# Kernel tuning notes

Measured on AMD Instinct MI355X. Metric: run time of the kernel, lower is better.

## Reference

```python
import jax, jax.numpy as jnp
import numpy as np

B, N, F, H, OUT, K, L = 32, 2048, 3, 64, 128, 16, 3


def _edge_mlp(e, w1, b1, wo, bo):
    # Faithful to the given MLP.forward: layer1 -> ReLU -> output (layer2 is skipped!)
    return jax.nn.relu(e @ w1 + b1) @ wo + bo


def _dynamic_edge_conv(x, k, w1, b1, wo, bo):
    # x: [B, N, D]. kNN in feature space (self included, distance 0), per graph.
    sq = jnp.sum(x * x, axis=-1)                                   # [B, N]
    d2 = sq[:, :, None] + sq[:, None, :] - 2.0 * jnp.einsum('bnd,bmd->bnm', x, x)
    _, idx = jax.lax.top_k(-d2, k)                                 # [B, N, K]
    x_j = jax.vmap(lambda xb, ib: xb[ib])(x, idx)                  # [B, N, K, D] gather
    x_i = jnp.broadcast_to(x[:, :, None, :], x_j.shape)
    e = jnp.concatenate([x_i, x_j - x_i], axis=-1)                 # EdgeConv message [B,N,K,2D]
    h = _edge_mlp(e, w1, b1, wo, bo)                               # [B, N, K, H]
    return jnp.mean(h, axis=2)                                     # aggr='mean' -> [B, N, H]


def setup_inputs() -> dict:
    key = jax.random.key(0)
    ks = jax.random.split(key, 20)
    inp = {'x': jax.random.normal(ks[0], (B, N, F), dtype=jnp.float32)}
    kit = iter(ks[1:])
    for i in range(L):
        din = 2 * F if i == 0 else 2 * H
        inp[f'w1_{i}'] = jax.random.normal(next(kit), (din, H), jnp.float32) / np.sqrt(din)
        inp[f'b1_{i}'] = jnp.zeros((H,), jnp.float32)
        inp[f'wo_{i}'] = jax.random.normal(next(kit), (H, H), jnp.float32) / np.sqrt(H)
        inp[f'bo_{i}'] = jnp.zeros((H,), jnp.float32)
    inp['fw1'] = jax.random.normal(next(kit), (H, H), jnp.float32) / np.sqrt(H)
    inp['fb1'] = jnp.zeros((H,), jnp.float32)
    inp['fw2'] = jax.random.normal(next(kit), (H, OUT), jnp.float32) / np.sqrt(H)
    inp['fb2'] = jnp.zeros((OUT,), jnp.float32)
    return inp


def reference(x, w1_0, b1_0, wo_0, bo_0, w1_1, b1_1, wo_1, bo_1, w1_2, b1_2, wo_2, bo_2, fw1, fb1, fw2, fb2):
    layers = [(w1_0, b1_0, wo_0, bo_0), (w1_1, b1_1, wo_1, bo_1), (w1_2, b1_2, wo_2, bo_2)]
    h = x
    for (w1, b1, wo, bo) in layers:
        h = _dynamic_edge_conv(h, K, w1, b1, wo, bo)
    g = jnp.mean(h, axis=1)                                        # global_mean_pool -> [B, H]
    return jax.nn.relu(g @ fw1 + fb1) @ fw2 + fb2                  # [B, OUT]
```

## Files before the change

kernel.cpp:

```cpp
#include <hip/hip_runtime.h>

#define BB 32
#define NN 2048
#define FF 3
#define HH 64
#define OUTC 128
#define KK 16
#define BN (BB * NN)

typedef __attribute__((ext_vector_type(8))) __bf16 bf16x8;
typedef __attribute__((ext_vector_type(4))) float f32x4;

__device__ __forceinline__ unsigned int packkey(float d2, unsigned int m) {
    unsigned int bb = __builtin_bit_cast(unsigned int, d2);
    unsigned int msk = (unsigned int)((int)bb >> 31);
    unsigned int srt = bb ^ (msk | 0x80000000u);
    return (srt & 0xFFFFF800u) | m;
}

__device__ __forceinline__ void ce(unsigned int& a, unsigned int& b) {
    unsigned int lo = a < b ? a : b;
    unsigned int hi = a < b ? b : a;
    a = lo; b = hi;
}

__device__ __forceinline__ void sort16(unsigned int k[16]) {
#pragma unroll
    for (int p = 1; p < 16; p <<= 1)
#pragma unroll
        for (int q = p; q >= 1; q >>= 1)
#pragma unroll
            for (int j = q % p; j + q < 16; j += 2 * q)
#pragma unroll
                for (int i = 0; i < q; ++i) {
                    int x = i + j, y = i + j + q;
                    if (y < 16 && (x / (2 * p) == y / (2 * p))) ce(k[x], k[y]);
                }
}

__device__ __forceinline__ void merge16(unsigned int keys[16], const unsigned int nk[16]) {
    unsigned int t[16];
#pragma unroll
    for (int i = 0; i < 16; ++i) {
        unsigned int b = nk[15 - i];
        t[i] = keys[i] < b ? keys[i] : b;
    }
#pragma unroll
    for (int d = 8; d >= 1; d >>= 1)
#pragma unroll
        for (int i = 0; i < 16; ++i)
            if ((i & d) == 0) ce(t[i], t[i ^ d]);
#pragma unroll
    for (int i = 0; i < 16; ++i) keys[i] = t[i];
}

__global__ __launch_bounds__(256) void prep3_kernel(const float* __restrict__ x,
                                                    const float* __restrict__ w1,
                                                    const float* __restrict__ b1,
                                                    float* __restrict__ sqo,
                                                    float* __restrict__ P,
                                                    float* __restrict__ Q) {
    const int tid = threadIdx.x;
    const int h = tid & 63;
    const int pl = tid >> 6;
    const long p = (long)blockIdx.x * 4 + pl;
    const float* fp = x + p * 3;
    const float f0 = fp[0], f1 = fp[1], f2 = fp[2];
    if (h == 0) sqo[p] = f0 * f0 + f1 * f1 + f2 * f2;
    float accp = 0.f, accq = 0.f;
    const float fv[3] = {f0, f1, f2};
#pragma unroll
    for (int d = 0; d < 3; ++d) {
        float wa = w1[d * HH + h];
        float wb = w1[(3 + d) * HH + h];
        accp = fmaf(fv[d], wa - wb, accp);
        accq = fmaf(fv[d], wb, accq);
    }
    P[p * HH + h] = accp + b1[h];
    Q[p * HH + h] = accq;
}

__global__ __launch_bounds__(256) void prep64_kernel(const float* __restrict__ feat,
                                                     const float* __restrict__ w1,
                                                     const float* __restrict__ b1,
                                                     __bf16* __restrict__ fbf,
                                                     float* __restrict__ sqo,
                                                     float* __restrict__ P,
                                                     float* __restrict__ Q) {
    __shared__ float rows[64 * HH];
    const int tid = threadIdx.x;
    const int h = tid & 63;
    const int wv = tid >> 6;
    const long row0 = (long)blockIdx.x * 64;

    float wdiff[64], wbv[64];
#pragma unroll
    for (int d = 0; d < 64; ++d) {
        float wa = w1[d * HH + h];
        float wb_ = w1[(HH + d) * HH + h];
        wdiff[d] = wa - wb_;
        wbv[d] = wb_;
    }
    const float bv = b1[h];

    {
        const float4* src = (const float4*)(feat + row0 * HH);
        float4* dst = (float4*)rows;
#pragma unroll
        for (int i = 0; i < 4; ++i) dst[tid + 256 * i] = src[tid + 256 * i];
    }
    __syncthreads();

    for (int r = wv * 16; r < wv * 16 + 16; ++r) {
        const long p = row0 + r;
        float fvh = rows[r * HH + h];
        fbf[p * HH + h] = (__bf16)fvh;
        float s = fvh * fvh;
        s += __shfl_xor(s, 1);
        s += __shfl_xor(s, 2);
        s += __shfl_xor(s, 4);
        s += __shfl_xor(s, 8);
        s += __shfl_xor(s, 16);
        s += __shfl_xor(s, 32);
        if (h == 0) sqo[p] = s;

        float ap0 = 0.f, ap1 = 0.f, aq0 = 0.f, aq1 = 0.f;
#pragma unroll
        for (int d4 = 0; d4 < 16; ++d4) {
            float4 fv = *(const float4*)&rows[r * HH + d4 * 4];
            ap0 = fmaf(fv.x, wdiff[4 * d4 + 0], ap0);
            aq0 = fmaf(fv.x, wbv[4 * d4 + 0], aq0);
            ap1 = fmaf(fv.y, wdiff[4 * d4 + 1], ap1);
            aq1 = fmaf(fv.y, wbv[4 * d4 + 1], aq1);
            ap0 = fmaf(fv.z, wdiff[4 * d4 + 2], ap0);
            aq0 = fmaf(fv.z, wbv[4 * d4 + 2], aq0);
            ap1 = fmaf(fv.w, wdiff[4 * d4 + 3], ap1);
            aq1 = fmaf(fv.w, wbv[4 * d4 + 3], aq1);
        }
        P[p * HH + h] = (ap0 + ap1) + bv;
        Q[p * HH + h] = aq0 + aq1;
    }
}

__global__ __launch_bounds__(256) void knn3_filter_kernel(const float* __restrict__ x,
                                                          const float* __restrict__ sq,
                                                          unsigned short* __restrict__ idx32) {
    __shared__ float4 lds_c[256];
    __shared__ unsigned int Km[64 * 68];
    const int tid = threadIdx.x;
    const int xcd = blockIdx.x & 7;
    const int ii = blockIdx.x >> 3;
    const int b = xcd + 8 * (ii >> 5);
    const int rg = ii & 31;
    const long pbase = (long)b * NN;
    const int r = tid >> 2, slot = tid & 3;
    const int row = rg * 64 + r;

    const float* rp = x + (pbase + row) * 3;
    const float xr0 = rp[0], xr1 = rp[1], xr2 = rp[2];

    unsigned int keys[KK];
#pragma unroll
    for (int j = 0; j < KK; ++j) keys[j] = 0xFFFFFFFFu;

    float c0, c1, c2, c3;
    {
        const float* cp = x + (pbase + tid) * 3;
        c0 = cp[0]; c1 = cp[1]; c2 = cp[2]; c3 = sq[pbase + tid];
    }

    for (int t = 0; t < NN / 256; ++t) {
        __syncthreads();
        lds_c[tid] = make_float4(c0, c1, c2, c3);
        __syncthreads();
        if (t < NN / 256 - 1) {
            const int m = (t + 1) * 256 + tid;
            const float* cp = x + (pbase + m) * 3;
            c0 = cp[0]; c1 = cp[1]; c2 = cp[2]; c3 = sq[pbase + m];
        }
        const int cbase = slot * 64;
#pragma unroll
        for (int bb = 0; bb < 4; ++bb) {
            unsigned int nk[16];
#pragma unroll
            for (int cc = 0; cc < 16; ++cc) {
                float4 v = lds_c[cbase + bb * 16 + cc];
                float dot = fmaf(xr0, v.x, fmaf(xr1, v.y, xr2 * v.z));
                float d2 = fmaf(-2.0f, dot, v.w);
                nk[cc] = packkey(d2, (unsigned int)(t * 256 + cbase + bb * 16 + cc));
            }
            sort16(nk);
            merge16(keys, nk);
        }
    }

    {
        uint4* kw = (uint4*)&Km[r * 68 + slot * 16];
#pragma unroll
        for (int q = 0; q < 4; ++q)
            kw[q] = make_uint4(keys[4 * q], keys[4 * q + 1], keys[4 * q + 2], keys[4 * q + 3]);
    }
    __syncthreads();
    if (slot < 2) {
        const unsigned int* k0 = &Km[r * 68 + slot * 32];
        const unsigned int* k1 = k0 + 16;
        unsigned short ms[16];
#pragma unroll
        for (int j = 0; j < 16; ++j) {
            unsigned int a = k0[j], bv = k1[15 - j];
            ms[j] = (unsigned short)((a < bv ? a : bv) & 0x7FFu);
        }
        uint4* op = (uint4*)(idx32 + ((pbase + row) * 32 + slot * 16));
        op[0] = ((const uint4*)ms)[0];
        op[1] = ((const uint4*)ms)[1];
    }
}

#define APAD 80
#define DPAD 68

__global__ __launch_bounds__(256) void knn_filter_kernel(const __bf16* __restrict__ fbf,
                                                         const float* __restrict__ sq,
                                                         unsigned short* __restrict__ idx32) {
    __shared__ __align__(16) __bf16 Ab[64 * APAD];
    __shared__ __align__(16) __bf16 Bb[64 * APAD];
    __shared__ __align__(16) unsigned int Dt[64 * DPAD];
    __shared__ float SqC[64];

    const int tid = threadIdx.x;
    const int xcd = blockIdx.x & 7;
    const int ii = blockIdx.x >> 3;
    const int b = xcd + 8 * (ii >> 5);
    const int rg = ii & 31;
    const long pbase = (long)b * NN;
    const int row0 = rg * 64;
    const int ci = tid >> 2, ch = tid & 3;

    {
        const __bf16* src = fbf + (pbase + row0 + ci) * 64 + ch * 16;
        uint4 v0 = *(const uint4*)src;
        uint4 v1 = *(const uint4*)(src + 8);
        *(uint4*)&Ab[ci * APAD + ch * 16] = v0;
        *(uint4*)&Ab[ci * APAD + ch * 16 + 8] = v1;
    }
    __syncthreads();

    const int wv = tid >> 6, ln = tid & 63;
    const int n16 = ln & 15, quad = ln >> 4;
    bf16x8 af0, af1;
    {
        const __bf16* ap = &Ab[(wv * 16 + n16) * APAD + quad * 8];
        af0 = *(const bf16x8*)ap;
        af1 = *(const bf16x8*)(ap + 32);
    }

    const int r = tid >> 2, slot = tid & 3;
    unsigned int keys[KK];
#pragma unroll
    for (int j = 0; j < KK; ++j) keys[j] = 0xFFFFFFFFu;

    uint4 pv0, pv1;
    float psq;
    {
        const __bf16* src = fbf + (pbase + ci) * 64 + ch * 16;
        pv0 = *(const uint4*)src;
        pv1 = *(const uint4*)(src + 8);
        psq = (tid < 64) ? sq[pbase + tid] : 0.f;
    }

    for (int t = 0; t < NN / 64; ++t) {
        *(uint4*)&Bb[ci * APAD + ch * 16] = pv0;
        *(uint4*)&Bb[ci * APAD + ch * 16 + 8] = pv1;
        if (tid < 64) SqC[tid] = psq;
        __syncthreads();

#pragma unroll
        for (int ct = 0; ct < 4; ++ct) {
            const __bf16* bp = &Bb[(ct * 16 + n16) * APAD + quad * 8];
            bf16x8 bf0 = *(const bf16x8*)bp;
            bf16x8 bf1 = *(const bf16x8*)(bp + 32);
            f32x4 acc = {0.f, 0.f, 0.f, 0.f};
            acc = __builtin_amdgcn_mfma_f32_16x16x32_bf16(af0, bf0, acc, 0, 0, 0);
            acc = __builtin_amdgcn_mfma_f32_16x16x32_bf16(af1, bf1, acc, 0, 0, 0);
            const int ccol = ct * 16 + n16;
            const float sqc = SqC[ccol];
            const unsigned int m = (unsigned int)(t * 64 + ccol);
#pragma unroll
            for (int rr = 0; rr < 4; ++rr) {
                const int rrow = wv * 16 + quad * 4 + rr;
                Dt[rrow * DPAD + ccol] = packkey(fmaf(-2.0f, acc[rr], sqc), m);
            }
        }
        __syncthreads();

        if (t < NN / 64 - 1) {
            const __bf16* src = fbf + (pbase + (long)(t + 1) * 64 + ci) * 64 + ch * 16;
            pv0 = *(const uint4*)src;
            pv1 = *(const uint4*)(src + 8);
            if (tid < 64) psq = sq[pbase + (t + 1) * 64 + tid];
        }

        {
            const uint4* kp = (const uint4*)&Dt[r * DPAD + slot * 16];
            unsigned int nk[16];
#pragma unroll
            for (int q = 0; q < 4; ++q) {
                uint4 kv = kp[q];
                nk[4 * q + 0] = kv.x; nk[4 * q + 1] = kv.y;
                nk[4 * q + 2] = kv.z; nk[4 * q + 3] = kv.w;
            }
            sort16(nk);
            merge16(keys, nk);
        }
    }

    __syncthreads();
    {
        uint4* kw = (uint4*)&Dt[r * DPAD + slot * 16];
#pragma unroll
        for (int q = 0; q < 4; ++q)
            kw[q] = make_uint4(keys[4 * q], keys[4 * q + 1], keys[4 * q + 2], keys[4 * q + 3]);
    }
    __syncthreads();
    if (slot < 2) {
        const unsigned int* k0 = &Dt[r * DPAD + slot * 32];
        const unsigned int* k1 = k0 + 16;
        unsigned short ms[16];
#pragma unroll
        for (int j = 0; j < 16; ++j) {
            unsigned int a = k0[j], bv = k1[15 - j];
            ms[j] = (unsigned short)((a < bv ? a : bv) & 0x7FFu);
        }
        uint4* op = (uint4*)(idx32 + ((pbase + row0 + r) * 32 + slot * 16));
        op[0] = ((const uint4*)ms)[0];
        op[1] = ((const uint4*)ms)[1];
    }
}

template <int D>
__global__ __launch_bounds__(256) void rescore_gather_kernel(const float* __restrict__ feat,
                                                             const float* __restrict__ sq,
                                                             const unsigned short* __restrict__ idx32,
                                                             const float* __restrict__ P,
                                                             const float* __restrict__ Q,
                                                             const float* __restrict__ wo,
                                                             const float* __restrict__ bo,
                                                             float* __restrict__ outf) {
    __shared__ float rowf[8][D];
    __shared__ float Sc[8][32];
    __shared__ int Ji[8][32];
    __shared__ float Sq32[8][32];
    __shared__ int Li[8][KK];
    __shared__ float Rl[8][HH];
    const int tid = threadIdx.x;
    const int w = tid >> 6, ln = tid & 63;
    const int rw = ln >> 5, c = ln & 31;
    const int xcd = blockIdx.x & 7;
    const int ii = blockIdx.x >> 3;
    const int batch = xcd + 8 * (ii >> 8);
    const int rb = ii & 255;
    const long pbase = (long)batch * NN;
    const long pblk = pbase + (long)rb * 8;
    const long p = pblk + w * 2 + rw;
    const int row_ = w * 2 + rw;

    for (int i = tid; i < 8 * D; i += 256) rowf[i / D][i % D] = feat[pblk * D + i];
    {
        const int j0 = (int)idx32[p * 32 + c];
        Ji[row_][c] = j0;
        Sq32[row_][c] = sq[pbase + j0];
    }
    __syncthreads();

    if constexpr (D == 64) {
        const int cg = ln >> 2, e = ln & 3;
#pragma unroll
        for (int rr = 0; rr < 2; ++rr) {
#pragma unroll
            for (int pp = 0; pp < 2; ++pp) {
                const int row = w * 2 + rr;
                const int cand = pp * 16 + cg;
                const int jj = Ji[row][cand];
                const float* cb = feat + (pbase + jj) * 64;
                float part = 0.f;
#pragma unroll
                for (int blk = 0; blk < 4; ++blk) {
                    float4 cv = *(const float4*)(cb + blk * 16 + e * 4);
                    float4 rv = *(const float4*)&rowf[row][blk * 16 + e * 4];
                    part = fmaf(rv.x, cv.x, part);
                    part = fmaf(rv.y, cv.y, part);
                    part = fmaf(rv.z, cv.z, part);
                    part = fmaf(rv.w, cv.w, part);
                }
                part += __shfl_xor(part, 1);
                part += __shfl_xor(part, 2);
                if (e == 0) Sc[row][cand] = fmaf(-2.0f, part, Sq32[row][cand]);
            }
        }
    } else {
        const int jj = Ji[row_][c];
        const float* cp = feat + (pbase + jj) * 3;
        float dot = fmaf(rowf[row_][0], cp[0],
                    fmaf(rowf[row_][1], cp[1], rowf[row_][2] * cp[2]));
        Sc[row_][c] = fmaf(-2.0f, dot, Sq32[row_][c]);
    }
    __syncthreads();

    {
        const float score = Sc[row_][c];
        const int j = Ji[row_][c];
        int rank = 0;
#pragma unroll
        for (int m = 0; m < 32; ++m) {
            float dm = Sc[row_][m];
            int jm = Ji[row_][m];
            rank += (dm < score || (dm == score && jm < j)) ? 1 : 0;
        }
        if (rank < KK) Li[row_][rank] = j;
    }
    __syncthreads();

    const int h = tid & 63, pl = tid >> 6;
#pragma unroll
    for (int rr0 = 0; rr0 < 2; ++rr0) {
        const int rr = pl + rr0 * 4;
        const long pp = pblk + rr;
        const float Pv = P[pp * HH + h];
        float acc = 0.f;
#pragma unroll
        for (int k = 0; k < KK; ++k) {
            int j2 = Li[rr][k];
            acc += fmaxf(Pv + Q[(pbase + j2) * HH + h], 0.f);
        }
        Rl[rr][h] = acc * (1.f / KK);
    }
    __syncthreads();
#pragma unroll
    for (int rr0 = 0; rr0 < 2; ++rr0) {
        const int rr = pl + rr0 * 4;
        float o = bo[h];
#pragma unroll
        for (int l = 0; l < HH; ++l) o = fmaf(Rl[rr][l], wo[l * HH + h], o);
        outf[(pblk + rr) * HH + h] = o;
    }
}

__global__ __launch_bounds__(256) void pool_partial_kernel(const float* __restrict__ feat,
                                                           float* __restrict__ pp) {
    __shared__ float part[4][HH];
    const int batch = blockIdx.x >> 3;
    const int chk = blockIdx.x & 7;
    const int tid = threadIdx.x;
    const int h = tid & 63;
    const int sub = tid >> 6;
    float s = 0.f;
    const float* fp = feat + ((long)batch * NN + chk * 256 + sub * 64) * HH + h;
    for (int n = 0; n < 64; ++n) s += fp[(long)n * HH];
    part[sub][h] = s;
    __syncthreads();
    if (tid < HH)
        pp[(batch * 8 + chk) * HH + h] = part[0][h] + part[1][h] + part[2][h] + part[3][h];
}

__global__ __launch_bounds__(256) void head_kernel(const float* __restrict__ pp,
                                                   const float* __restrict__ fw1,
                                                   const float* __restrict__ fb1,
                                                   const float* __restrict__ fw2,
                                                   const float* __restrict__ fb2,
                                                   float* __restrict__ out) {
    __shared__ float g[HH];
    __shared__ float tl[HH];
    const int b = blockIdx.x;
    const int tid = threadIdx.x;
    if (tid < HH) {
        float s = 0.f;
#pragma unroll
        for (int c = 0; c < 8; ++c) s += pp[(b * 8 + c) * HH + tid];
        g[tid] = s * (1.f / NN);
    }
    __syncthreads();
    if (tid < HH) {
        float a = fb1[tid];
#pragma unroll
        for (int l = 0; l < HH; ++l) a = fmaf(g[l], fw1[l * HH + tid], a);
        tl[tid] = fmaxf(a, 0.f);
    }
    __syncthreads();
    if (tid < OUTC) {
        float o = fb2[tid];
#pragma unroll
        for (int l = 0; l < HH; ++l) o = fmaf(tl[l], fw2[l * OUTC + tid], o);
        out[(long)b * OUTC + tid] = o;
    }
}

extern "C" void kernel_launch(void* const* d_in, const int* in_sizes, int n_in,
                              void* d_out, int out_size, void* d_ws, size_t ws_size,
                              hipStream_t stream) {
    const float* x    = (const float*)d_in[0];
    const float* w1_0 = (const float*)d_in[1];
    const float* b1_0 = (const float*)d_in[2];
    const float* wo_0 = (const float*)d_in[3];
    const float* bo_0 = (const float*)d_in[4];
    const float* w1_1 = (const float*)d_in[5];
    const float* b1_1 = (const float*)d_in[6];
    const float* wo_1 = (const float*)d_in[7];
    const float* bo_1 = (const float*)d_in[8];
    const float* w1_2 = (const float*)d_in[9];
    const float* b1_2 = (const float*)d_in[10];
    const float* wo_2 = (const float*)d_in[11];
    const float* bo_2 = (const float*)d_in[12];
    const float* fw1  = (const float*)d_in[13];
    const float* fb1  = (const float*)d_in[14];
    const float* fw2  = (const float*)d_in[15];
    const float* fb2  = (const float*)d_in[16];
    float* out = (float*)d_out;

    float* featA = (float*)d_ws;
    float* featB = featA + (long)BN * HH;
    float* Pb    = featB + (long)BN * HH;
    float* Qb    = Pb + (long)BN * HH;
    float* sqb   = Qb + (long)BN * HH;
    unsigned short* idx32 = (unsigned short*)(sqb + BN);
    float* ppb   = (float*)(idx32 + (long)BN * 32);

    __bf16* fbf1 = (__bf16*)featB;
    __bf16* fbf2 = (__bf16*)featA;

    prep3_kernel<<<BN / 4, 256, 0, stream>>>(x, w1_0, b1_0, sqb, Pb, Qb);
    knn3_filter_kernel<<<BB * 32, 256, 0, stream>>>(x, sqb, idx32);
    rescore_gather_kernel<3><<<BN / 8, 256, 0, stream>>>(x, sqb, idx32, Pb, Qb, wo_0, bo_0, featA);

    prep64_kernel<<<BN / 64, 256, 0, stream>>>(featA, w1_1, b1_1, fbf1, sqb, Pb, Qb);
    knn_filter_kernel<<<BB * 32, 256, 0, stream>>>(fbf1, sqb, idx32);
    rescore_gather_kernel<64><<<BN / 8, 256, 0, stream>>>(featA, sqb, idx32, Pb, Qb, wo_1, bo_1, featB);

    prep64_kernel<<<BN / 64, 256, 0, stream>>>(featB, w1_2, b1_2, fbf2, sqb, Pb, Qb);
    knn_filter_kernel<<<BB * 32, 256, 0, stream>>>(fbf2, sqb, idx32);
    rescore_gather_kernel<64><<<BN / 8, 256, 0, stream>>>(featB, sqb, idx32, Pb, Qb, wo_2, bo_2, featA);

    pool_partial_kernel<<<BB * 8, 256, 0, stream>>>(featA, ppb);
    head_kernel<<<BB, 256, 0, stream>>>(ppb, fw1, fb1, fw2, fb2, out);
}
```

Baseline: 614.5 us.

## Fuse prep into kNN and rescore kernels, drop bf16 copy and pool kernel

Merges the layer-0 P/Q prep into the first kNN kernel as extra blocks, and computes squared norms inside the preceding rescore kernel rather than the prep kernels. The kNN filter now reads fp32 features and converts to bf16 in-kernel, so the separate bf16 feature copy goes away. The last layer's rescore writes per-block partial sums directly, removing the pool kernel and the final feature write. The aim is fewer launches and less global traffic. The cost is that the kNN kernel reads twice as many bytes and does in-loop conversion, and the head kernel reduces more partial sums.

```diff
diff --git a/kernel.cpp b/kernel.cpp
--- a/kernel.cpp
+++ b/kernel.cpp
@@ -54,39 +54,114 @@
     for (int i = 0; i < 16; ++i) keys[i] = t[i];
 }
 
-__global__ __launch_bounds__(256) void prep3_kernel(const float* __restrict__ x,
+__device__ __forceinline__ unsigned short bfbits(float v) {
+    return __builtin_bit_cast(unsigned short, (__bf16)v);
+}
+
+__global__ __launch_bounds__(256) void pack3_kernel(const float* __restrict__ x,
                                                     const float* __restrict__ w1,
                                                     const float* __restrict__ b1,
-                                                    float* __restrict__ sqo,
                                                     float* __restrict__ P,
-                                                    float* __restrict__ Q) {
+                                                    float* __restrict__ Q,
+                                                    unsigned short* __restrict__ idx32) {
+    __shared__ float4 lds_c[256];
+    __shared__ unsigned int Km[64 * 68];
     const int tid = threadIdx.x;
-    const int h = tid & 63;
-    const int pl = tid >> 6;
-    const long p = (long)blockIdx.x * 4 + pl;
-    const float* fp = x + p * 3;
-    const float f0 = fp[0], f1 = fp[1], f2 = fp[2];
-    if (h == 0) sqo[p] = f0 * f0 + f1 * f1 + f2 * f2;
-    float accp = 0.f, accq = 0.f;
-    const float fv[3] = {f0, f1, f2};
-#pragma unroll
-    for (int d = 0; d < 3; ++d) {
-        float wa = w1[d * HH + h];
-        float wb = w1[(3 + d) * HH + h];
-        accp = fmaf(fv[d], wa - wb, accp);
-        accq = fmaf(fv[d], wb, accq);
-    }
-    P[p * HH + h] = accp + b1[h];
-    Q[p * HH + h] = accq;
-}
-
-__global__ __launch_bounds__(256) void prep64_kernel(const float* __restrict__ feat,
-                                                     const float* __restrict__ w1,
-                                                     const float* __restrict__ b1,
-                                                     __bf16* __restrict__ fbf,
-                                                     float* __restrict__ sqo,
-                                                     float* __restrict__ P,
-                                                     float* __restrict__ Q) {
+
+    if (blockIdx.x >= 1024) {
+        const int h = tid & 63;
+        const int pl = tid >> 6;
+        const long p = (long)(blockIdx.x - 1024) * 4 + pl;
+        const float* fp = x + p * 3;
+        const float fv[3] = {fp[0], fp[1], fp[2]};
+        float accp = 0.f, accq = 0.f;
+#pragma unroll
+        for (int d = 0; d < 3; ++d) {
+            float wa = w1[d * HH + h];
+            float wb = w1[(3 + d) * HH + h];
+            accp = fmaf(fv[d], wa - wb, accp);
+            accq = fmaf(fv[d], wb, accq);
+        }
+        P[p * HH + h] = accp + b1[h];
+        Q[p * HH + h] = accq;
+        return;
+    }
+
+    const int xcd = blockIdx.x & 7;
+    const int ii = blockIdx.x >> 3;
+    const int b = xcd + 8 * (ii >> 5);
+    const int rg = ii & 31;
+    const long pbase = (long)b * NN;
+    const int r = tid >> 2, slot = tid & 3;
+    const int row = rg * 64 + r;
+
+    const float* rp = x + (pbase + row) * 3;
+    const float xr0 = rp[0], xr1 = rp[1], xr2 = rp[2];
+
+    unsigned int keys[KK];
+#pragma unroll
+    for (int j = 0; j < KK; ++j) keys[j] = 0xFFFFFFFFu;
+
+    float c0, c1, c2, c3;
+    {
+        const float* cp = x + (pbase + tid) * 3;
+        c0 = cp[0]; c1 = cp[1]; c2 = cp[2];
+        c3 = c0 * c0 + c1 * c1 + c2 * c2;
+    }
+
+    for (int t = 0; t < NN / 256; ++t) {
+        __syncthreads();
+        lds_c[tid] = make_float4(c0, c1, c2, c3);
+        __syncthreads();
+        if (t < NN / 256 - 1) {
+            const int m = (t + 1) * 256 + tid;
+            const float* cp = x + (pbase + m) * 3;
+            c0 = cp[0]; c1 = cp[1]; c2 = cp[2];
+            c3 = c0 * c0 + c1 * c1 + c2 * c2;
+        }
+        const int cbase = slot * 64;
+#pragma unroll
+        for (int bb = 0; bb < 4; ++bb) {
+            unsigned int nk[16];
+#pragma unroll
+            for (int cc = 0; cc < 16; ++cc) {
+                float4 v = lds_c[cbase + bb * 16 + cc];
+                float dot = fmaf(xr0, v.x, fmaf(xr1, v.y, xr2 * v.z));
+                float d2 = fmaf(-2.0f, dot, v.w);
+                nk[cc] = packkey(d2, (unsigned int)(t * 256 + cbase + bb * 16 + cc));
+            }
+            sort16(nk);
+            merge16(keys, nk);
+        }
+    }
+
+    {
+        uint4* kw = (uint4*)&Km[r * 68 + slot * 16];
+#pragma unroll
+        for (int q = 0; q < 4; ++q)
+            kw[q] = make_uint4(keys[4 * q], keys[4 * q + 1], keys[4 * q + 2], keys[4 * q + 3]);
+    }
+    __syncthreads();
+    if (slot < 2) {
+        const unsigned int* k0 = &Km[r * 68 + slot * 32];
+        const unsigned int* k1 = k0 + 16;
+        unsigned short ms[16];
+#pragma unroll
+        for (int j = 0; j < 16; ++j) {
+            unsigned int a = k0[j], bv = k1[15 - j];
+            ms[j] = (unsigned short)((a < bv ? a : bv) & 0x7FFu);
+        }
+        uint4* op = (uint4*)(idx32 + ((pbase + row) * 32 + slot * 16));
+        op[0] = ((const uint4*)ms)[0];
+        op[1] = ((const uint4*)ms)[1];
+    }
+}
+
+__global__ __launch_bounds__(256) void prep_pq64_kernel(const float* __restrict__ feat,
+                                                        const float* __restrict__ w1,
+                                                        const float* __restrict__ b1,
+                                                        float* __restrict__ P,
+                                                        float* __restrict__ Q) {
     __shared__ float rows[64 * HH];
     const int tid = threadIdx.x;
     const int h = tid & 63;
@@ -113,17 +188,6 @@
 
     for (int r = wv * 16; r < wv * 16 + 16; ++r) {
         const long p = row0 + r;
-        float fvh = rows[r * HH + h];
-        fbf[p * HH + h] = (__bf16)fvh;
-        float s = fvh * fvh;
-        s += __shfl_xor(s, 1);
-        s += __shfl_xor(s, 2);
-        s += __shfl_xor(s, 4);
-        s += __shfl_xor(s, 8);
-        s += __shfl_xor(s, 16);
-        s += __shfl_xor(s, 32);
-        if (h == 0) sqo[p] = s;
-
         float ap0 = 0.f, ap1 = 0.f, aq0 = 0.f, aq1 = 0.f;
 #pragma unroll
         for (int d4 = 0; d4 < 16; ++d4) {
@@ -142,84 +206,10 @@
     }
 }
 
-__global__ __launch_bounds__(256) void knn3_filter_kernel(const float* __restrict__ x,
-                                                          const float* __restrict__ sq,
-                                                          unsigned short* __restrict__ idx32) {
-    __shared__ float4 lds_c[256];
-    __shared__ unsigned int Km[64 * 68];
-    const int tid = threadIdx.x;
-    const int xcd = blockIdx.x & 7;
-    const int ii = blockIdx.x >> 3;
-    const int b = xcd + 8 * (ii >> 5);
-    const int rg = ii & 31;
-    const long pbase = (long)b * NN;
-    const int r = tid >> 2, slot = tid & 3;
-    const int row = rg * 64 + r;
-
-    const float* rp = x + (pbase + row) * 3;
-    const float xr0 = rp[0], xr1 = rp[1], xr2 = rp[2];
-
-    unsigned int keys[KK];
-#pragma unroll
-    for (int j = 0; j < KK; ++j) keys[j] = 0xFFFFFFFFu;
-
-    float c0, c1, c2, c3;
-    {
-        const float* cp = x + (pbase + tid) * 3;
-        c0 = cp[0]; c1 = cp[1]; c2 = cp[2]; c3 = sq[pbase + tid];
-    }
-
-    for (int t = 0; t < NN / 256; ++t) {
-        __syncthreads();
-        lds_c[tid] = make_float4(c0, c1, c2, c3);
-        __syncthreads();
-        if (t < NN / 256 - 1) {
-            const int m = (t + 1) * 256 + tid;
-            const float* cp = x + (pbase + m) * 3;
-            c0 = cp[0]; c1 = cp[1]; c2 = cp[2]; c3 = sq[pbase + m];
-        }
-        const int cbase = slot * 64;
-#pragma unroll
-        for (int bb = 0; bb < 4; ++bb) {
-            unsigned int nk[16];
-#pragma unroll
-            for (int cc = 0; cc < 16; ++cc) {
-                float4 v = lds_c[cbase + bb * 16 + cc];
-                float dot = fmaf(xr0, v.x, fmaf(xr1, v.y, xr2 * v.z));
-                float d2 = fmaf(-2.0f, dot, v.w);
-                nk[cc] = packkey(d2, (unsigned int)(t * 256 + cbase + bb * 16 + cc));
-            }
-            sort16(nk);
-            merge16(keys, nk);
-        }
-    }
-
-    {
-        uint4* kw = (uint4*)&Km[r * 68 + slot * 16];
-#pragma unroll
-        for (int q = 0; q < 4; ++q)
-            kw[q] = make_uint4(keys[4 * q], keys[4 * q + 1], keys[4 * q + 2], keys[4 * q + 3]);
-    }
-    __syncthreads();
-    if (slot < 2) {
-        const unsigned int* k0 = &Km[r * 68 + slot * 32];
-        const unsigned int* k1 = k0 + 16;
-        unsigned short ms[16];
-#pragma unroll
-        for (int j = 0; j < 16; ++j) {
-            unsigned int a = k0[j], bv = k1[15 - j];
-            ms[j] = (unsigned short)((a < bv ? a : bv) & 0x7FFu);
-        }
-        uint4* op = (uint4*)(idx32 + ((pbase + row) * 32 + slot * 16));
-        op[0] = ((const uint4*)ms)[0];
-        op[1] = ((const uint4*)ms)[1];
-    }
-}
-
 #define APAD 80
 #define DPAD 68
 
-__global__ __launch_bounds__(256) void knn_filter_kernel(const __bf16* __restrict__ fbf,
+__global__ __launch_bounds__(256) void knn_filter_kernel(const float* __restrict__ feat,
                                                          const float* __restrict__ sq,
                                                          unsigned short* __restrict__ idx32) {
     __shared__ __align__(16) __bf16 Ab[64 * APAD];
@@ -234,14 +224,17 @@
     const int rg = ii & 31;
     const long pbase = (long)b * NN;
     const int row0 = rg * 64;
-    const int ci = tid >> 2, ch = tid & 3;
-
-    {
-        const __bf16* src = fbf + (pbase + row0 + ci) * 64 + ch * 16;
-        uint4 v0 = *(const uint4*)src;
-        uint4 v1 = *(const uint4*)(src + 8);
-        *(uint4*)&Ab[ci * APAD + ch * 16] = v0;
-        *(uint4*)&Ab[ci * APAD + ch * 16 + 8] = v1;
+
+    {
+        const float4* src = (const float4*)(feat + (pbase + row0) * 64);
+#pragma unroll
+        for (int it = 0; it < 4; ++it) {
+            const int i = it * 256 + tid;
+            float4 v = src[i];
+            const int rw = i >> 4, col = (i & 15) * 4;
+            unsigned short u[4] = {bfbits(v.x), bfbits(v.y), bfbits(v.z), bfbits(v.w)};
+            *(uint2*)&Ab[rw * APAD + col] = *(const uint2*)u;
+        }
     }
     __syncthreads();
 
@@ -259,18 +252,24 @@
 #pragma unroll
     for (int j = 0; j < KK; ++j) keys[j] = 0xFFFFFFFFu;
 
-    uint4 pv0, pv1;
+    float4 pv[4];
     float psq;
     {
-        const __bf16* src = fbf + (pbase + ci) * 64 + ch * 16;
-        pv0 = *(const uint4*)src;
-        pv1 = *(const uint4*)(src + 8);
+        const float4* src = (const float4*)(feat + pbase * 64);
+#pragma unroll
+        for (int it = 0; it < 4; ++it) pv[it] = src[it * 256 + tid];
         psq = (tid < 64) ? sq[pbase + tid] : 0.f;
     }
 
     for (int t = 0; t < NN / 64; ++t) {
-        *(uint4*)&Bb[ci * APAD + ch * 16] = pv0;
-        *(uint4*)&Bb[ci * APAD + ch * 16 + 8] = pv1;
+#pragma unroll
+        for (int it = 0; it < 4; ++it) {
+            const int i = it * 256 + tid;
+            const int rw = i >> 4, col = (i & 15) * 4;
+            unsigned short u[4] = {bfbits(pv[it].x), bfbits(pv[it].y),
+                                   bfbits(pv[it].z), bfbits(pv[it].w)};
+            *(uint2*)&Bb[rw * APAD + col] = *(const uint2*)u;
+        }
         if (tid < 64) SqC[tid] = psq;
         __syncthreads();
 
@@ -294,9 +293,9 @@
         __syncthreads();
 
         if (t < NN / 64 - 1) {
-            const __bf16* src = fbf + (pbase + (long)(t + 1) * 64 + ci) * 64 + ch * 16;
-            pv0 = *(const uint4*)src;
-            pv1 = *(const uint4*)(src + 8);
+            const float4* src = (const float4*)(feat + (pbase + (long)(t + 1) * 64) * 64);
+#pragma unroll
+            for (int it = 0; it < 4; ++it) pv[it] = src[it * 256 + tid];
             if (tid < 64) psq = sq[pbase + (t + 1) * 64 + tid];
         }
 
@@ -337,19 +336,17 @@
     }
 }
 
-template <int D>
-__global__ __launch_bounds__(256) void rescore_gather_kernel(const float* __restrict__ feat,
-                                                             const float* __restrict__ sq,
-                                                             const unsigned short* __restrict__ idx32,
-                                                             const float* __restrict__ P,
-                                                             const float* __restrict__ Q,
-                                                             const float* __restrict__ wo,
-                                                             const float* __restrict__ bo,
-                                                             float* __restrict__ outf) {
-    __shared__ float rowf[8][D];
+__global__ __launch_bounds__(256) void rescore3_kernel(const float* __restrict__ x,
+                                                       const unsigned short* __restrict__ idx32,
+                                                       const float* __restrict__ P,
+                                                       const float* __restrict__ Q,
+                                                       const float* __restrict__ wo,
+                                                       const float* __restrict__ bo,
+                                                       float* __restrict__ outf,
+                                                       float* __restrict__ sqn) {
+    __shared__ float rowf[8][3];
     __shared__ float Sc[8][32];
     __shared__ int Ji[8][32];
-    __shared__ float Sq32[8][32];
     __shared__ int Li[8][KK];
     __shared__ float Rl[8][HH];
     const int tid = threadIdx.x;
@@ -364,7 +361,98 @@
     const long p = pblk + w * 2 + rw;
     const int row_ = w * 2 + rw;
 
-    for (int i = tid; i < 8 * D; i += 256) rowf[i / D][i % D] = feat[pblk * D + i];
+    for (int i = tid; i < 24; i += 256) rowf[i / 3][i % 3] = x[pblk * 3 + i];
+    Ji[row_][c] = (int)idx32[p * 32 + c];
+    __syncthreads();
+
+    {
+        const int jj = Ji[row_][c];
+        const float* cp = x + (pbase + jj) * 3;
+        const float c0 = cp[0], c1 = cp[1], c2 = cp[2];
+        const float sqc = c0 * c0 + c1 * c1 + c2 * c2;
+        float dot = fmaf(rowf[row_][0], c0, fmaf(rowf[row_][1], c1, rowf[row_][2] * c2));
+        Sc[row_][c] = fmaf(-2.0f, dot, sqc);
+    }
+    __syncthreads();
+
+    {
+        const float score = Sc[row_][c];
+        const int j = Ji[row_][c];
+        int rank = 0;
+#pragma unroll
+        for (int m = 0; m < 32; ++m) {
+            float dm = Sc[row_][m];
+            int jm = Ji[row_][m];
+            rank += (dm < score || (dm == score && jm < j)) ? 1 : 0;
+        }
+        if (rank < KK) Li[row_][rank] = j;
+    }
+    __syncthreads();
+
+    const int h = tid & 63, pl = tid >> 6;
+#pragma unroll
+    for (int rr0 = 0; rr0 < 2; ++rr0) {
+        const int rr = pl + rr0 * 4;
+        const long pp = pblk + rr;
+        const float Pv = P[pp * HH + h];
+        float acc = 0.f;
+#pragma unroll
+        for (int k = 0; k < KK; ++k) {
+            int j2 = Li[rr][k];
+            acc += fmaxf(Pv + Q[(pbase + j2) * HH + h], 0.f);
+        }
+        Rl[rr][h] = acc * (1.f / KK);
+    }
+    __syncthreads();
+#pragma unroll
+    for (int rr0 = 0; rr0 < 2; ++rr0) {
+        const int rr = pl + rr0 * 4;
+        float o = bo[h];
+#pragma unroll
+        for (int l = 0; l < HH; ++l) o = fmaf(Rl[rr][l], wo[l * HH + h], o);
+        outf[(pblk + rr) * HH + h] = o;
+        float s2 = o * o;
+        s2 += __shfl_xor(s2, 1);
+        s2 += __shfl_xor(s2, 2);
+        s2 += __shfl_xor(s2, 4);
+        s2 += __shfl_xor(s2, 8);
+        s2 += __shfl_xor(s2, 16);
+        s2 += __shfl_xor(s2, 32);
+        if (h == 0) sqn[pblk + rr] = s2;
+    }
+}
+
+template <bool LAST>
+__global__ __launch_bounds__(256) void rescore64_kernel(const float* __restrict__ feat,
+                                                        const float* __restrict__ sq,
+                                                        const unsigned short* __restrict__ idx32,
+                                                        const float* __restrict__ P,
+                                                        const float* __restrict__ Q,
+                                                        const float* __restrict__ wo,
+                                                        const float* __restrict__ bo,
+                                                        float* __restrict__ outf,
+                                                        float* __restrict__ sqn,
+                                                        float* __restrict__ ppb) {
+    __shared__ float rowf[8][HH];
+    __shared__ float Sc[8][32];
+    __shared__ int Ji[8][32];
+    __shared__ float Sq32[8][32];
+    __shared__ int Li[8][KK];
+    __shared__ float Rl[8][HH];
+    __shared__ float Psum[4][HH];
+    const int tid = threadIdx.x;
+    const int w = tid >> 6, ln = tid & 63;
+    const int rw = ln >> 5, c = ln & 31;
+    const int xcd = blockIdx.x & 7;
+    const int ii = blockIdx.x >> 3;
+    const int batch = xcd + 8 * (ii >> 8);
+    const int rb = ii & 255;
+    const long pbase = (long)batch * NN;
+    const long pblk = pbase + (long)rb * 8;
+    const long p = pblk + w * 2 + rw;
+    const int row_ = w * 2 + rw;
+
+    for (int i = tid; i < 8 * HH; i += 256) rowf[i / HH][i % HH] = feat[pblk * HH + i];
     {
         const int j0 = (int)idx32[p * 32 + c];
         Ji[row_][c] = j0;
@@ -372,7 +460,7 @@
     }
     __syncthreads();
 
-    if constexpr (D == 64) {
+    {
         const int cg = ln >> 2, e = ln & 3;
 #pragma unroll
         for (int rr = 0; rr < 2; ++rr) {
@@ -397,12 +485,6 @@
                 if (e == 0) Sc[row][cand] = fmaf(-2.0f, part, Sq32[row][cand]);
             }
         }
-    } else {
-        const int jj = Ji[row_][c];
-        const float* cp = feat + (pbase + jj) * 3;
-        float dot = fmaf(rowf[row_][0], cp[0],
-                    fmaf(rowf[row_][1], cp[1], rowf[row_][2] * cp[2]));
-        Sc[row_][c] = fmaf(-2.0f, dot, Sq32[row_][c]);
     }
     __syncthreads();
 
@@ -435,49 +517,56 @@
         Rl[rr][h] = acc * (1.f / KK);
     }
     __syncthreads();
+
+    float posum = 0.f;
 #pragma unroll
     for (int rr0 = 0; rr0 < 2; ++rr0) {
         const int rr = pl + rr0 * 4;
         float o = bo[h];
 #pragma unroll
         for (int l = 0; l < HH; ++l) o = fmaf(Rl[rr][l], wo[l * HH + h], o);
-        outf[(pblk + rr) * HH + h] = o;
-    }
-}
-
-__global__ __launch_bounds__(256) void pool_partial_kernel(const float* __restrict__ feat,
-                                                           float* __restrict__ pp) {
-    __shared__ float part[4][HH];
-    const int batch = blockIdx.x >> 3;
-    const int chk = blockIdx.x & 7;
-    const int tid = threadIdx.x;
-    const int h = tid & 63;
-    const int sub = tid >> 6;
-    float s = 0.f;
-    const float* fp = feat + ((long)batch * NN + chk * 256 + sub * 64) * HH + h;
-    for (int n = 0; n < 64; ++n) s += fp[(long)n * HH];
-    part[sub][h] = s;
-    __syncthreads();
-    if (tid < HH)
-        pp[(batch * 8 + chk) * HH + h] = part[0][h] + part[1][h] + part[2][h] + part[3][h];
-}
-
-__global__ __launch_bounds__(256) void head_kernel(const float* __restrict__ pp,
+        if constexpr (!LAST) {
+            outf[(pblk + rr) * HH + h] = o;
+            float s2 = o * o;
+            s2 += __shfl_xor(s2, 1);
+            s2 += __shfl_xor(s2, 2);
+            s2 += __shfl_xor(s2, 4);
+            s2 += __shfl_xor(s2, 8);
+            s2 += __shfl_xor(s2, 16);
+            s2 += __shfl_xor(s2, 32);
+            if (h == 0) sqn[pblk + rr] = s2;
+        } else {
+            posum += o;
+        }
+    }
+    if constexpr (LAST) {
+        Psum[pl][h] = posum;
+        __syncthreads();
+        if (tid < HH) {
+            float t4 = Psum[0][tid] + Psum[1][tid] + Psum[2][tid] + Psum[3][tid];
+            ppb[((long)batch * 256 + rb) * HH + tid] = t4;
+        }
+    }
+}
+
+__global__ __launch_bounds__(256) void head_kernel(const float* __restrict__ ppb,
                                                    const float* __restrict__ fw1,
                                                    const float* __restrict__ fb1,
                                                    const float* __restrict__ fw2,
                                                    const float* __restrict__ fb2,
                                                    float* __restrict__ out) {
+    __shared__ float part[4][HH];
     __shared__ float g[HH];
     __shared__ float tl[HH];
     const int b = blockIdx.x;
     const int tid = threadIdx.x;
-    if (tid < HH) {
-        float s = 0.f;
-#pragma unroll
-        for (int c = 0; c < 8; ++c) s += pp[(b * 8 + c) * HH + tid];
-        g[tid] = s * (1.f / NN);
-    }
+    const int h = tid & 63;
+    const int ck = tid >> 6;
+    float s = 0.f;
+    for (int i = ck; i < 256; i += 4) s += ppb[((long)b * 256 + i) * HH + h];
+    part[ck][h] = s;
+    __syncthreads();
+    if (tid < HH) g[tid] = (part[0][tid] + part[1][tid] + part[2][tid] + part[3][tid]) * (1.f / NN);
     __syncthreads();
     if (tid < HH) {
         float a = fb1[tid];
@@ -520,25 +609,23 @@
     float* featB = featA + (long)BN * HH;
     float* Pb    = featB + (long)BN * HH;
     float* Qb    = Pb + (long)BN * HH;
-    float* sqb   = Qb + (long)BN * HH;
-    unsigned short* idx32 = (unsigned short*)(sqb + BN);
+    float* sqA   = Qb + (long)BN * HH;
+    float* sqB   = sqA + BN;
+    unsigned short* idx32 = (unsigned short*)(sqB + BN);
     float* ppb   = (float*)(idx32 + (long)BN * 32);
 
-    __bf16* fbf1 = (__bf16*)featB;
-    __bf16* fbf2 = (__bf16*)featA;
-
-    prep3_kernel<<<BN / 4, 256, 0, stream>>>(x, w1_0, b1_0, sqb, Pb, Qb);
-    knn3_filter_kernel<<<BB * 32, 256, 0, stream>>>(x, sqb, idx32);
-    rescore_gather_kernel<3><<<BN / 8, 256, 0, stream>>>(x, sqb, idx32, Pb, Qb, wo_0, bo_0, featA);
-
-    prep64_kernel<<<BN / 64, 256, 0, stream>>>(featA, w1_1, b1_1, fbf1, sqb, Pb, Qb);
-    knn_filter_kernel<<<BB * 32, 256, 0, stream>>>(fbf1, sqb, idx32);
-    rescore_gather_kernel<64><<<BN / 8, 256, 0, stream>>>(featA, sqb, idx32, Pb, Qb, wo_1, bo_1, featB);
-
-    prep64_kernel<<<BN / 64, 256, 0, stream>>>(featB, w1_2, b1_2, fbf2, sqb, Pb, Qb);
-    knn_filter_kernel<<<BB * 32, 256, 0, stream>>>(fbf2, sqb, idx32);
-    rescore_gather_kernel<64><<<BN / 8, 256, 0, stream>>>(featB, sqb, idx32, Pb, Qb, wo_2, bo_2, featA);
-
-    pool_partial_kernel<<<BB * 8, 256, 0, stream>>>(featA, ppb);
+    pack3_kernel<<<1024 + BN / 4, 256, 0, stream>>>(x, w1_0, b1_0, Pb, Qb, idx32);
+    rescore3_kernel<<<BN / 8, 256, 0, stream>>>(x, idx32, Pb, Qb, wo_0, bo_0, featA, sqB);
+
+    prep_pq64_kernel<<<BN / 64, 256, 0, stream>>>(featA, w1_1, b1_1, Pb, Qb);
+    knn_filter_kernel<<<BB * 32, 256, 0, stream>>>(featA, sqB, idx32);
+    rescore64_kernel<false><<<BN / 8, 256, 0, stream>>>(featA, sqB, idx32, Pb, Qb, wo_1, bo_1,
+                                                        featB, sqA, nullptr);
+
+    prep_pq64_kernel<<<BN / 64, 256, 0, stream>>>(featB, w1_2, b1_2, Pb, Qb);
+    knn_filter_kernel<<<BB * 32, 256, 0, stream>>>(featB, sqA, idx32);
+    rescore64_kernel<true><<<BN / 8, 256, 0, stream>>>(featB, sqA, idx32, Pb, Qb, wo_2, bo_2,
+                                                       nullptr, nullptr, ppb);
+
     head_kernel<<<BB, 256, 0, stream>>>(ppb, fw1, fb1, fw2, fb2, out);
 }
```

Result: slower. 669.4 us (+8.9%).
